# Optimization experiments

Measured on AMD Instinct MI355X. Metric: run time of the kernel, lower is better.

Reference implementation:

```python
import jax, jax.numpy as jnp
import numpy as np

B, S, D, H = 2, 2048, 1024, 16
HD = D // H  # 64
SCALE = float(np.sqrt(HD))


def setup_inputs() -> dict:
    key = jax.random.key(0)
    ks = jax.random.split(key, 5)
    x = jax.random.normal(ks[0], (B, S, D), dtype=jnp.float32)
    # causal mask: 1 = attend, 0 = masked
    mask = jnp.tril(jnp.ones((S, S), dtype=jnp.int32))
    xavier = lambda k: jax.random.normal(k, (D, D), dtype=jnp.float32) * np.sqrt(2.0 / (D + D))
    return {
        "x": x,
        "mask": mask,
        "Wq": xavier(ks[1]),
        "Wk": xavier(ks[2]),
        "Wv": xavier(ks[3]),
        "Wo": xavier(ks[4]),
    }


def reference(x, mask, Wq, Wk, Wv, Wo):
    # torch Linear(bias=False): y = x @ W.T  with W of shape [out, in]
    def heads(W):
        return (x @ W.T).reshape(B, S, H, HD).transpose(0, 2, 1, 3)  # [B,H,S,HD]

    Q, K, V = heads(Wq), heads(Wk), heads(Wv)
    scores = jnp.einsum("bhqd,bhkd->bhqk", Q, K) / SCALE  # [B,H,S,S]
    scores = jnp.where(mask[None, None] == 0, -jnp.inf, scores)
    attn = jax.nn.softmax(scores, axis=-1)
    attn = jnp.where(jnp.isnan(attn), jnp.zeros_like(attn), attn)  # nan-fix for fully masked rows
    # dropout is identity in eval / p=0
    out = jnp.einsum("bhqk,bhkd->bhqd", attn, V)  # [B,H,S,HD]
    out = out.transpose(0, 2, 1, 3).reshape(B, S, D)
    return out @ Wo.T
```

## Files before the change

### kernel.cpp

```cpp
#include <hip/hip_runtime.h>


using bfx8 = __attribute__((ext_vector_type(8))) short;
using bfx4 = __attribute__((ext_vector_type(4))) short;
using fx4  = __attribute__((ext_vector_type(4))) float;

#define NB 2
#define NS 2048
#define ND 1024
#define NH 16
#define NHD 64
#define LSTR 72

__device__ __forceinline__ unsigned short f2bf(float f) {
  union { float f; unsigned u; } v; v.f = f;
  return (unsigned short)((v.u + 0x7fffu + ((v.u >> 16) & 1u)) >> 16);
}
__device__ __forceinline__ unsigned pk2(float a, float b) {
  return (unsigned)f2bf(a) | ((unsigned)f2bf(b) << 16);
}

#define GLD16(gp, lp) __builtin_amdgcn_global_load_lds( \
    (__attribute__((address_space(1))) void*)(gp),      \
    (__attribute__((address_space(3))) void*)(lp), 16, 0, 0)

__global__ __launch_bounds__(256)
void cvt_all(const float4* __restrict__ x,  const float4* __restrict__ wq,
             const float4* __restrict__ wk, const float4* __restrict__ wv,
             const float4* __restrict__ wo, unsigned short* __restrict__ dst) {
  const int NT4 = (NB * NS * ND) / 4, NW4 = (ND * ND) / 4;
  const int i = blockIdx.x * 256 + threadIdx.x;
  const float4* src;
  int off;
  if (i < NT4) {
    src = x; off = i;
  } else {
    const int k = i - NT4;
    const int seg = k / NW4;
    off = k - seg * NW4;
    src = (seg == 0) ? wq : (seg == 1) ? wk : (seg == 2) ? wv : wo;
  }
  float4 f = src[off];
  uint2 w;
  w.x = pk2(f.x, f.y);
  w.y = pk2(f.z, f.w);
  *(uint2*)(dst + (size_t)i * 4) = w;
}

template <bool BF16>
__global__ __launch_bounds__(256)
void gemm_qkv(const void* __restrict__ xv,
              const void* __restrict__ W0v, const void* __restrict__ W1v,
              const void* __restrict__ W2v,
              unsigned short* __restrict__ Qb, unsigned short* __restrict__ Kb,
              unsigned short* __restrict__ Vt, float SCL) {
  __shared__ __attribute__((aligned(16))) unsigned short As[128 * 32];
  __shared__ __attribute__((aligned(16))) unsigned short Bs[128 * 32];
  const int t = threadIdx.x;
  const int lane = t & 63, wave = t >> 6;
  const int wr = wave >> 1, wc = wave & 1;
  const int r16 = lane & 15, quad = lane >> 4;
  const int m0 = blockIdx.x * 128, n0 = blockIdx.y * 128;
  const int z = blockIdx.z;
  const void* Wv = (z == 0) ? W0v : (z == 1) ? W1v : W2v;
  const int KD = 1024;
  fx4 acc[4][4] = {};
  const int row2 = t >> 1, kh = t & 1;
  const int c0 = t, c1 = t + 256;

  for (int k0 = 0; k0 < KD; k0 += 32) {
    if constexpr (BF16) {
      const unsigned short* A = (const unsigned short*)xv;
      const unsigned short* W = (const unsigned short*)Wv;
      GLD16(A + (size_t)(m0 + (c0 >> 2)) * KD + (size_t)(c0 & 3) * 8 + k0, &As[c0 * 8]);
      GLD16(A + (size_t)(m0 + (c1 >> 2)) * KD + (size_t)(c1 & 3) * 8 + k0, &As[c1 * 8]);
      GLD16(W + (size_t)(n0 + (c0 >> 2)) * KD + (size_t)(c0 & 3) * 8 + k0, &Bs[c0 * 8]);
      GLD16(W + (size_t)(n0 + (c1 >> 2)) * KD + (size_t)(c1 & 3) * 8 + k0, &Bs[c1 * 8]);
    } else {
      const float* A = (const float*)xv;
      const float* W = (const float*)Wv;
      {
        const float4* src = (const float4*)(A + (size_t)(m0 + row2) * KD + k0 + kh * 16);
        float4 f0 = src[0], f1 = src[1], f2 = src[2], f3 = src[3];
        uint4 w0 = {pk2(f0.x, f0.y), pk2(f0.z, f0.w), pk2(f1.x, f1.y), pk2(f1.z, f1.w)};
        uint4 w1 = {pk2(f2.x, f2.y), pk2(f2.z, f2.w), pk2(f3.x, f3.y), pk2(f3.z, f3.w)};
        *(uint4*)&As[row2 * 32 + kh * 16] = w0;
        *(uint4*)&As[row2 * 32 + kh * 16 + 8] = w1;
      }
      {
        const float4* src = (const float4*)(W + (size_t)(n0 + row2) * KD + k0 + kh * 16);
        float4 f0 = src[0], f1 = src[1], f2 = src[2], f3 = src[3];
        uint4 w0 = {pk2(f0.x, f0.y), pk2(f0.z, f0.w), pk2(f1.x, f1.y), pk2(f1.z, f1.w)};
        uint4 w1 = {pk2(f2.x, f2.y), pk2(f2.z, f2.w), pk2(f3.x, f3.y), pk2(f3.z, f3.w)};
        *(uint4*)&Bs[row2 * 32 + kh * 16] = w0;
        *(uint4*)&Bs[row2 * 32 + kh * 16 + 8] = w1;
      }
    }
    __syncthreads();
    bfx8 af[4], bfr[4];
#pragma unroll
    for (int mt = 0; mt < 4; mt++)
      af[mt] = *(const bfx8*)&As[(wr * 64 + mt * 16 + r16) * 32 + quad * 8];
#pragma unroll
    for (int nt = 0; nt < 4; nt++)
      bfr[nt] = *(const bfx8*)&Bs[(wc * 64 + nt * 16 + r16) * 32 + quad * 8];
#pragma unroll
    for (int mt = 0; mt < 4; mt++)
#pragma unroll
      for (int nt = 0; nt < 4; nt++)
        acc[mt][nt] = __builtin_amdgcn_mfma_f32_16x16x32_bf16(
            af[mt], bfr[nt], acc[mt][nt], 0, 0, 0);
    __syncthreads();
  }
#pragma unroll
  for (int mt = 0; mt < 4; mt++) {
#pragma unroll
    for (int nt = 0; nt < 4; nt++) {
      fx4 v = acc[mt][nt];
      const int mb = m0 + wr * 64 + mt * 16 + quad * 4;
      const int n = n0 + wc * 64 + nt * 16 + r16;
      const int b = mb >> 11, s = mb & (NS - 1);
      const int h = n >> 6, hd = n & (NHD - 1);
      if (z <= 1) {
        unsigned short* C = (z == 0) ? Qb : Kb;
        const float sc = (z == 0) ? SCL : 1.0f;
        const size_t base = ((size_t)(b * NH + h) * NS + s) * NHD + hd;
#pragma unroll
        for (int r = 0; r < 4; r++) C[base + (size_t)r * NHD] = f2bf(v[r] * sc);
      } else {
        const size_t base = ((size_t)(b * NH + h) * NHD + hd) * NS + s;
        uint2 pw;
        pw.x = pk2(v[0], v[1]);
        pw.y = pk2(v[2], v[3]);
        *(uint2*)(Vt + base) = pw;
      }
    }
  }
}

template <bool BF16>
__global__ __launch_bounds__(256)
void gemm_out(const unsigned short* __restrict__ A,
              const void* __restrict__ Wv,
              float* __restrict__ C) {
  __shared__ __attribute__((aligned(16))) unsigned short As[128 * 32];
  __shared__ __attribute__((aligned(16))) unsigned short Bs[128 * 32];
  const int t = threadIdx.x;
  const int lane = t & 63, wave = t >> 6;
  const int wr = wave >> 1, wc = wave & 1;
  const int r16 = lane & 15, quad = lane >> 4;
  const int m0 = blockIdx.x * 128, n0 = blockIdx.y * 128;
  const int KD = 1024;
  fx4 acc[4][4] = {};
  const int row2 = t >> 1, kh = t & 1;
  const int c0 = t, c1 = t + 256;
  for (int k0 = 0; k0 < KD; k0 += 32) {
    GLD16(A + (size_t)(m0 + (c0 >> 2)) * KD + (size_t)(c0 & 3) * 8 + k0, &As[c0 * 8]);
    GLD16(A + (size_t)(m0 + (c1 >> 2)) * KD + (size_t)(c1 & 3) * 8 + k0, &As[c1 * 8]);
    if constexpr (BF16) {
      const unsigned short* W = (const unsigned short*)Wv;
      GLD16(W + (size_t)(n0 + (c0 >> 2)) * KD + (size_t)(c0 & 3) * 8 + k0, &Bs[c0 * 8]);
      GLD16(W + (size_t)(n0 + (c1 >> 2)) * KD + (size_t)(c1 & 3) * 8 + k0, &Bs[c1 * 8]);
    } else {
      const float* W = (const float*)Wv;
      const float4* src = (const float4*)(W + (size_t)(n0 + row2) * KD + k0 + kh * 16);
      float4 f0 = src[0], f1 = src[1], f2 = src[2], f3 = src[3];
      uint4 w0 = {pk2(f0.x, f0.y), pk2(f0.z, f0.w), pk2(f1.x, f1.y), pk2(f1.z, f1.w)};
      uint4 w1 = {pk2(f2.x, f2.y), pk2(f2.z, f2.w), pk2(f3.x, f3.y), pk2(f3.z, f3.w)};
      *(uint4*)&Bs[row2 * 32 + kh * 16] = w0;
      *(uint4*)&Bs[row2 * 32 + kh * 16 + 8] = w1;
    }
    __syncthreads();
    bfx8 af[4], bfr[4];
#pragma unroll
    for (int mt = 0; mt < 4; mt++)
      af[mt] = *(const bfx8*)&As[(wr * 64 + mt * 16 + r16) * 32 + quad * 8];
#pragma unroll
    for (int nt = 0; nt < 4; nt++)
      bfr[nt] = *(const bfx8*)&Bs[(wc * 64 + nt * 16 + r16) * 32 + quad * 8];
#pragma unroll
    for (int mt = 0; mt < 4; mt++)
#pragma unroll
      for (int nt = 0; nt < 4; nt++)
        acc[mt][nt] = __builtin_amdgcn_mfma_f32_16x16x32_bf16(
            af[mt], bfr[nt], acc[mt][nt], 0, 0, 0);
    __syncthreads();
  }
#pragma unroll
  for (int mt = 0; mt < 4; mt++) {
#pragma unroll
    for (int nt = 0; nt < 4; nt++) {
      fx4 v = acc[mt][nt];
      const int s = m0 + wr * 64 + mt * 16 + quad * 4;
      const int n = n0 + wc * 64 + nt * 16 + r16;
      const size_t base = (size_t)s * ND + n;
#pragma unroll
      for (int r = 0; r < 4; r++) C[base + (size_t)r * ND] = v[r];
    }
  }
}

__global__ __launch_bounds__(256)
void attn_mfma(const unsigned short* __restrict__ Q,
               const unsigned short* __restrict__ K,
               const unsigned short* __restrict__ Vt,
               unsigned short* __restrict__ O) {
  __shared__ __attribute__((aligned(16))) unsigned short Ks[64 * LSTR];
  __shared__ __attribute__((aligned(16))) unsigned short Vs[64 * LSTR];
  const int t = threadIdx.x;
  const int lane = t & 63, wave = t >> 6;
  const int r16 = lane & 15, quad = lane >> 4;
  const int bh = blockIdx.x;
  const int j = blockIdx.y;
  const int tile = (j < 8) ? j : 23 - j;
  const int b = bh >> 4, h = bh & (NH - 1);
  const int q0b = tile * 128;
  const int q0w = q0b + wave * 32;
  const int nT = (q0b + 128) >> 6;
  const unsigned short* Qp = Q + (size_t)bh * NS * NHD;
  const unsigned short* Kp = K + (size_t)bh * NS * NHD;
  const unsigned short* Vp = Vt + (size_t)bh * NHD * NS;

  bfx8 qf[2][2];
#pragma unroll
  for (int qt = 0; qt < 2; qt++)
#pragma unroll
    for (int hs = 0; hs < 2; hs++)
      qf[qt][hs] = *(const bfx8*)&Qp[(size_t)(q0w + qt * 16 + r16) * NHD + hs * 32 + quad * 8];

  fx4 acc[2][4] = {};
  float lsum[2] = {0.0f, 0.0f};

  const int c0 = t, c1 = t + 256;
  uint4 kr0 = *(const uint4*)&Kp[0 * 64 + 8 * c0];
  uint4 kr1 = *(const uint4*)&Kp[0 * 64 + 8 * c1];
  uint4 vr0 = *(const uint4*)&Vp[(size_t)(c0 >> 3) * NS + 0 + (c0 & 7) * 8];
  uint4 vr1 = *(const uint4*)&Vp[(size_t)(c1 >> 3) * NS + 0 + (c1 & 7) * 8];

  for (int tt = 0; tt < nT; tt++) {
    __syncthreads();
    *(uint4*)&Ks[(c0 >> 3) * LSTR + (c0 & 7) * 8] = kr0;
    *(uint4*)&Ks[(c1 >> 3) * LSTR + (c1 & 7) * 8] = kr1;
    *(uint4*)&Vs[(c0 >> 3) * LSTR + (c0 & 7) * 8] = vr0;
    *(uint4*)&Vs[(c1 >> 3) * LSTR + (c1 & 7) * 8] = vr1;
    if (tt + 1 < nT) {
      const int kk = (tt + 1) * 64;
      kr0 = *(const uint4*)&Kp[kk * 64 + 8 * c0];
      kr1 = *(const uint4*)&Kp[kk * 64 + 8 * c1];
      vr0 = *(const uint4*)&Vp[(size_t)(c0 >> 3) * NS + kk + (c0 & 7) * 8];
      vr1 = *(const uint4*)&Vp[(size_t)(c1 >> 3) * NS + kk + (c1 & 7) * 8];
    }
    __syncthreads();

#pragma unroll
    for (int ks32 = 0; ks32 < 2; ks32++) {
      const int kkeff = tt * 64 + ks32 * 32;
      if (kkeff > q0w) break;
      bfx8 kf[2][2];
      bfx4 vf[4][2];
#pragma unroll
      for (int kt = 0; kt < 2; kt++)
#pragma unroll
        for (int hs = 0; hs < 2; hs++)
          kf[kt][hs] = *(const bfx8*)&Ks[(ks32 * 32 + kt * 16 + r16) * LSTR + hs * 32 + quad * 8];
#pragma unroll
      for (int mt = 0; mt < 4; mt++)
#pragma unroll
        for (int ks = 0; ks < 2; ks++)
          vf[mt][ks] = *(const bfx4*)&Vs[(mt * 16 + r16) * LSTR + ks32 * 32 + ks * 16 + quad * 4];

      fx4 st[2][2] = {};
#pragma unroll
      for (int kt = 0; kt < 2; kt++)
#pragma unroll
        for (int qt = 0; qt < 2; qt++)
#pragma unroll
          for (int hs = 0; hs < 2; hs++)
            st[kt][qt] = __builtin_amdgcn_mfma_f32_16x16x32_bf16(
                kf[kt][hs], qf[qt][hs], st[kt][qt], 0, 0, 0);

      if (kkeff == q0w) {
#pragma unroll
        for (int kt = 0; kt < 2; kt++)
#pragma unroll
          for (int qt = 0; qt < 2; qt++) {
            const int query = q0w + qt * 16 + r16;
#pragma unroll
            for (int r = 0; r < 4; r++) {
              const int key = kkeff + kt * 16 + quad * 4 + r;
              if (key > query) st[kt][qt][r] = -1e30f;
            }
          }
      }

#pragma unroll
      for (int qt = 0; qt < 2; qt++) {
        float p[2][4];
        float ps = 0.0f;
#pragma unroll
        for (int kt = 0; kt < 2; kt++)
#pragma unroll
          for (int r = 0; r < 4; r++) {
            p[kt][r] = exp2f(st[kt][qt][r]);
            ps += p[kt][r];
          }
        lsum[qt] += ps;
        uint4 pbu;
        pbu.x = pk2(p[0][0], p[0][1]);
        pbu.y = pk2(p[0][2], p[0][3]);
        pbu.z = pk2(p[1][0], p[1][1]);
        pbu.w = pk2(p[1][2], p[1][3]);
        bfx8 pb = *(bfx8*)&pbu;
#pragma unroll
        for (int mt = 0; mt < 4; mt++) {
          bfx8 va = __builtin_shufflevector(vf[mt][0], vf[mt][1], 0, 1, 2, 3, 4, 5, 6, 7);
          acc[qt][mt] = __builtin_amdgcn_mfma_f32_16x16x32_bf16(
              va, pb, acc[qt][mt], 0, 0, 0);
        }
      }
    }
  }

#pragma unroll
  for (int qt = 0; qt < 2; qt++) {
    float l = lsum[qt];
    l += __shfl_xor(l, 16);
    l += __shfl_xor(l, 32);
    const float rinv = 1.0f / l;
    const int s = q0w + qt * 16 + r16;
#pragma unroll
    for (int mt = 0; mt < 4; mt++) {
      const int d = h * NHD + mt * 16 + quad * 4;
      uint2 pw;
      pw.x = pk2(acc[qt][mt][0] * rinv, acc[qt][mt][1] * rinv);
      pw.y = pk2(acc[qt][mt][2] * rinv, acc[qt][mt][3] * rinv);
      *(uint2*)(O + ((size_t)b * NS + s) * ND + d) = pw;
    }
  }
}

extern "C" void kernel_launch(void* const* d_in, const int* in_sizes, int n_in,
                              void* d_out, int out_size, void* d_ws, size_t ws_size,
                              hipStream_t stream) {
  const float* x  = (const float*)d_in[0];
  const float* Wq = (const float*)d_in[2];
  const float* Wk = (const float*)d_in[3];
  const float* Wv = (const float*)d_in[4];
  const float* Wo = (const float*)d_in[5];
  float* out = (float*)d_out;
  unsigned short* ws = (unsigned short*)d_ws;
  const float QSCL = 0.125f * 1.44269504f;
  dim3 blk(256);
  const size_t NT = (size_t)NB * NS * ND;
  const size_t NW = (size_t)ND * ND;

  if (ws_size >= (size_t)48 * 1024 * 1024) {
    unsigned short* xb  = ws;
    unsigned short* Wqb = ws + NT;
    unsigned short* Wkb = ws + NT + NW;
    unsigned short* Wvb = ws + NT + 2 * NW;
    unsigned short* Wob = ws + NT + 3 * NW;
    unsigned short* Qb  = ws + NT + 4 * NW;
    unsigned short* Kb  = Qb + NT;
    unsigned short* Vt  = Qb + 2 * NT;
    unsigned short* Ob  = Qb + 3 * NT;
    const int total4 = (int)((NT + 4 * NW) / 4);
    hipLaunchKernelGGL(cvt_all, dim3(total4 / 256), blk, 0, stream,
                       (const float4*)x, (const float4*)Wq, (const float4*)Wk,
                       (const float4*)Wv, (const float4*)Wo, xb);
    hipLaunchKernelGGL((gemm_qkv<true>), dim3(32, 8, 3), blk, 0, stream,
                       xb, Wqb, Wkb, Wvb, Qb, Kb, Vt, QSCL);
    hipLaunchKernelGGL(attn_mfma, dim3(32, 16), blk, 0, stream, Qb, Kb, Vt, Ob);
    hipLaunchKernelGGL((gemm_out<true>), dim3(32, 8), blk, 0, stream, Ob, Wob, out);
  } else if (ws_size >= (size_t)32 * 1024 * 1024) {
    unsigned short* Qb = ws;
    unsigned short* Kb = ws + NT;
    unsigned short* Vt = ws + 2 * NT;
    unsigned short* Ob = ws + 3 * NT;
    hipLaunchKernelGGL((gemm_qkv<false>), dim3(32, 8, 3), blk, 0, stream,
                       x, Wq, Wk, Wv, Qb, Kb, Vt, QSCL);
    hipLaunchKernelGGL(attn_mfma, dim3(32, 16), blk, 0, stream, Qb, Kb, Vt, Ob);
    hipLaunchKernelGGL((gemm_out<false>), dim3(32, 8), blk, 0, stream, Ob, Wo, out);
  } else {
    const size_t NBA = (size_t)NS * ND;
    unsigned short* Qb = ws;
    unsigned short* Kb = ws + NBA;
    unsigned short* Vt = ws + 2 * NBA;
    unsigned short* Ob = ws + 3 * NBA;
    for (int b = 0; b < NB; b++) {
      const float* xb = x + (size_t)b * NS * ND;
      float* ob = out + (size_t)b * NS * ND;
      hipLaunchKernelGGL((gemm_qkv<false>), dim3(16, 8, 3), blk, 0, stream,
                         xb, Wq, Wk, Wv, Qb, Kb, Vt, QSCL);
      hipLaunchKernelGGL(attn_mfma, dim3(16, 16), blk, 0, stream, Qb, Kb, Vt, Ob);
      hipLaunchKernelGGL((gemm_out<false>), dim3(16, 8), blk, 0, stream, Ob, Wo, ob);
    }
  }
}
```

Baseline: 215.4 us.

## Transpose QKV GEMM over concatenated weights, truncate P to bf16, reorder attention tiles

The QKV projection becomes a single GEMM over the concatenated bf16 weights (which are already contiguous in the workspace), computing W·xᵀ so that each lane's four accumulator values run along the feature dimension. This lets Q and K be written as packed 8-byte stores instead of scattered scalar stores. The attention kernel now schedules query tiles heaviest-first and packs the probabilities to bf16 by truncation instead of round-to-nearest, which saves ALU work but adds a small rounding bias. The fp32 fallback path is split into its own kernel with unchanged logic.

```diff
diff --git a/kernel.cpp b/kernel.cpp
--- a/kernel.cpp
+++ b/kernel.cpp
@@ -18,6 +18,10 @@
 }
 __device__ __forceinline__ unsigned pk2(float a, float b) {
   return (unsigned)f2bf(a) | ((unsigned)f2bf(b) << 16);
+}
+__device__ __forceinline__ unsigned pkt(float a, float b) {
+  union { float f; unsigned u; } ua, ub; ua.f = a; ub.f = b;
+  return (ua.u >> 16) | (ub.u & 0xffff0000u);
 }
 
 #define GLD16(gp, lp) __builtin_amdgcn_global_load_lds( \
@@ -47,13 +51,84 @@
   *(uint2*)(dst + (size_t)i * 4) = w;
 }
 
-template <bool BF16>
 __global__ __launch_bounds__(256)
-void gemm_qkv(const void* __restrict__ xv,
-              const void* __restrict__ W0v, const void* __restrict__ W1v,
-              const void* __restrict__ W2v,
-              unsigned short* __restrict__ Qb, unsigned short* __restrict__ Kb,
-              unsigned short* __restrict__ Vt, float SCL) {
+void gemm_qkvT(const unsigned short* __restrict__ Wcat,
+               const unsigned short* __restrict__ xb,
+               unsigned short* __restrict__ Qb, unsigned short* __restrict__ Kb,
+               unsigned short* __restrict__ Vt, float SCL) {
+  __shared__ __attribute__((aligned(16))) unsigned short As[128 * 32];
+  __shared__ __attribute__((aligned(16))) unsigned short Bs[128 * 32];
+  const int t = threadIdx.x;
+  const int lane = t & 63, wave = t >> 6;
+  const int wr = wave >> 1, wc = wave & 1;
+  const int r16 = lane & 15, quad = lane >> 4;
+  const int n0 = blockIdx.x * 128;
+  const int m0 = blockIdx.y * 128;
+  const int KD = 1024;
+  fx4 acc[4][4] = {};
+  const int c0 = t, c1 = t + 256;
+
+  for (int k0 = 0; k0 < KD; k0 += 32) {
+    GLD16(Wcat + (size_t)(n0 + (c0 >> 2)) * KD + (size_t)(c0 & 3) * 8 + k0, &As[c0 * 8]);
+    GLD16(Wcat + (size_t)(n0 + (c1 >> 2)) * KD + (size_t)(c1 & 3) * 8 + k0, &As[c1 * 8]);
+    GLD16(xb   + (size_t)(m0 + (c0 >> 2)) * KD + (size_t)(c0 & 3) * 8 + k0, &Bs[c0 * 8]);
+    GLD16(xb   + (size_t)(m0 + (c1 >> 2)) * KD + (size_t)(c1 & 3) * 8 + k0, &Bs[c1 * 8]);
+    __syncthreads();
+    bfx8 af[4], bfr[4];
+#pragma unroll
+    for (int ni = 0; ni < 4; ni++)
+      af[ni] = *(const bfx8*)&As[(wr * 64 + ni * 16 + r16) * 32 + quad * 8];
+#pragma unroll
+    for (int mi = 0; mi < 4; mi++)
+      bfr[mi] = *(const bfx8*)&Bs[(wc * 64 + mi * 16 + r16) * 32 + quad * 8];
+#pragma unroll
+    for (int ni = 0; ni < 4; ni++)
+#pragma unroll
+      for (int mi = 0; mi < 4; mi++)
+        acc[ni][mi] = __builtin_amdgcn_mfma_f32_16x16x32_bf16(
+            af[ni], bfr[mi], acc[ni][mi], 0, 0, 0);
+    __syncthreads();
+  }
+#pragma unroll
+  for (int ni = 0; ni < 4; ni++) {
+#pragma unroll
+    for (int mi = 0; mi < 4; mi++) {
+      fx4 v = acc[ni][mi];
+      const int n = n0 + wr * 64 + ni * 16 + quad * 4;
+      const int m = m0 + wc * 64 + mi * 16 + r16;
+      const int b = m >> 11, s = m & (NS - 1);
+      if (n0 < 1024) {
+        const int h = n >> 6, hd = n & (NHD - 1);
+        const size_t base = ((size_t)(b * NH + h) * NS + s) * NHD + hd;
+        uint2 pw;
+        pw.x = pk2(v[0] * SCL, v[1] * SCL);
+        pw.y = pk2(v[2] * SCL, v[3] * SCL);
+        *(uint2*)(Qb + base) = pw;
+      } else if (n0 < 2048) {
+        const int n2 = n - 1024;
+        const int h = n2 >> 6, hd = n2 & (NHD - 1);
+        const size_t base = ((size_t)(b * NH + h) * NS + s) * NHD + hd;
+        uint2 pw;
+        pw.x = pk2(v[0], v[1]);
+        pw.y = pk2(v[2], v[3]);
+        *(uint2*)(Kb + base) = pw;
+      } else {
+        const int n2 = n - 2048;
+        const int h = n2 >> 6, hd = n2 & (NHD - 1);
+        const size_t base = ((size_t)(b * NH + h) * NHD + hd) * NS + s;
+#pragma unroll
+        for (int r = 0; r < 4; r++) Vt[base + (size_t)r * NS] = f2bf(v[r]);
+      }
+    }
+  }
+}
+
+__global__ __launch_bounds__(256)
+void gemm_qkv_f32(const float* __restrict__ x,
+                  const float* __restrict__ W0, const float* __restrict__ W1,
+                  const float* __restrict__ W2,
+                  unsigned short* __restrict__ Qb, unsigned short* __restrict__ Kb,
+                  unsigned short* __restrict__ Vt, float SCL) {
   __shared__ __attribute__((aligned(16))) unsigned short As[128 * 32];
   __shared__ __attribute__((aligned(16))) unsigned short Bs[128 * 32];
   const int t = threadIdx.x;
@@ -62,39 +137,26 @@
   const int r16 = lane & 15, quad = lane >> 4;
   const int m0 = blockIdx.x * 128, n0 = blockIdx.y * 128;
   const int z = blockIdx.z;
-  const void* Wv = (z == 0) ? W0v : (z == 1) ? W1v : W2v;
+  const float* W = (z == 0) ? W0 : (z == 1) ? W1 : W2;
   const int KD = 1024;
   fx4 acc[4][4] = {};
   const int row2 = t >> 1, kh = t & 1;
-  const int c0 = t, c1 = t + 256;
-
   for (int k0 = 0; k0 < KD; k0 += 32) {
-    if constexpr (BF16) {
-      const unsigned short* A = (const unsigned short*)xv;
-      const unsigned short* W = (const unsigned short*)Wv;
-      GLD16(A + (size_t)(m0 + (c0 >> 2)) * KD + (size_t)(c0 & 3) * 8 + k0, &As[c0 * 8]);
-      GLD16(A + (size_t)(m0 + (c1 >> 2)) * KD + (size_t)(c1 & 3) * 8 + k0, &As[c1 * 8]);
-      GLD16(W + (size_t)(n0 + (c0 >> 2)) * KD + (size_t)(c0 & 3) * 8 + k0, &Bs[c0 * 8]);
-      GLD16(W + (size_t)(n0 + (c1 >> 2)) * KD + (size_t)(c1 & 3) * 8 + k0, &Bs[c1 * 8]);
-    } else {
-      const float* A = (const float*)xv;
-      const float* W = (const float*)Wv;
-      {
-        const float4* src = (const float4*)(A + (size_t)(m0 + row2) * KD + k0 + kh * 16);
-        float4 f0 = src[0], f1 = src[1], f2 = src[2], f3 = src[3];
-        uint4 w0 = {pk2(f0.x, f0.y), pk2(f0.z, f0.w), pk2(f1.x, f1.y), pk2(f1.z, f1.w)};
-        uint4 w1 = {pk2(f2.x, f2.y), pk2(f2.z, f2.w), pk2(f3.x, f3.y), pk2(f3.z, f3.w)};
-        *(uint4*)&As[row2 * 32 + kh * 16] = w0;
-        *(uint4*)&As[row2 * 32 + kh * 16 + 8] = w1;
-      }
-      {
-        const float4* src = (const float4*)(W + (size_t)(n0 + row2) * KD + k0 + kh * 16);
-        float4 f0 = src[0], f1 = src[1], f2 = src[2], f3 = src[3];
-        uint4 w0 = {pk2(f0.x, f0.y), pk2(f0.z, f0.w), pk2(f1.x, f1.y), pk2(f1.z, f1.w)};
-        uint4 w1 = {pk2(f2.x, f2.y), pk2(f2.z, f2.w), pk2(f3.x, f3.y), pk2(f3.z, f3.w)};
-        *(uint4*)&Bs[row2 * 32 + kh * 16] = w0;
-        *(uint4*)&Bs[row2 * 32 + kh * 16 + 8] = w1;
-      }
+    {
+      const float4* src = (const float4*)(x + (size_t)(m0 + row2) * KD + k0 + kh * 16);
+      float4 f0 = src[0], f1 = src[1], f2 = src[2], f3 = src[3];
+      uint4 w0 = {pk2(f0.x, f0.y), pk2(f0.z, f0.w), pk2(f1.x, f1.y), pk2(f1.z, f1.w)};
+      uint4 w1 = {pk2(f2.x, f2.y), pk2(f2.z, f2.w), pk2(f3.x, f3.y), pk2(f3.z, f3.w)};
+      *(uint4*)&As[row2 * 32 + kh * 16] = w0;
+      *(uint4*)&As[row2 * 32 + kh * 16 + 8] = w1;
+    }
+    {
+      const float4* src = (const float4*)(W + (size_t)(n0 + row2) * KD + k0 + kh * 16);
+      float4 f0 = src[0], f1 = src[1], f2 = src[2], f3 = src[3];
+      uint4 w0 = {pk2(f0.x, f0.y), pk2(f0.z, f0.w), pk2(f1.x, f1.y), pk2(f1.z, f1.w)};
+      uint4 w1 = {pk2(f2.x, f2.y), pk2(f2.z, f2.w), pk2(f3.x, f3.y), pk2(f3.z, f3.w)};
+      *(uint4*)&Bs[row2 * 32 + kh * 16] = w0;
+      *(uint4*)&Bs[row2 * 32 + kh * 16 + 8] = w1;
     }
     __syncthreads();
     bfx8 af[4], bfr[4];
@@ -211,8 +273,7 @@
   const int lane = t & 63, wave = t >> 6;
   const int r16 = lane & 15, quad = lane >> 4;
   const int bh = blockIdx.x;
-  const int j = blockIdx.y;
-  const int tile = (j < 8) ? j : 23 - j;
+  const int tile = 15 - blockIdx.y;
   const int b = bh >> 4, h = bh & (NH - 1);
   const int q0b = tile * 128;
   const int q0w = q0b + wave * 32;
@@ -232,10 +293,10 @@
   float lsum[2] = {0.0f, 0.0f};
 
   const int c0 = t, c1 = t + 256;
-  uint4 kr0 = *(const uint4*)&Kp[0 * 64 + 8 * c0];
-  uint4 kr1 = *(const uint4*)&Kp[0 * 64 + 8 * c1];
-  uint4 vr0 = *(const uint4*)&Vp[(size_t)(c0 >> 3) * NS + 0 + (c0 & 7) * 8];
-  uint4 vr1 = *(const uint4*)&Vp[(size_t)(c1 >> 3) * NS + 0 + (c1 & 7) * 8];
+  uint4 kr0 = *(const uint4*)&Kp[8 * c0];
+  uint4 kr1 = *(const uint4*)&Kp[8 * c1];
+  uint4 vr0 = *(const uint4*)&Vp[(size_t)(c0 >> 3) * NS + (c0 & 7) * 8];
+  uint4 vr1 = *(const uint4*)&Vp[(size_t)(c1 >> 3) * NS + (c1 & 7) * 8];
 
   for (int tt = 0; tt < nT; tt++) {
     __syncthreads();
@@ -306,10 +367,10 @@
           }
         lsum[qt] += ps;
         uint4 pbu;
-        pbu.x = pk2(p[0][0], p[0][1]);
-        pbu.y = pk2(p[0][2], p[0][3]);
-        pbu.z = pk2(p[1][0], p[1][1]);
-        pbu.w = pk2(p[1][2], p[1][3]);
+        pbu.x = pkt(p[0][0], p[0][1]);
+        pbu.y = pkt(p[0][2], p[0][3]);
+        pbu.z = pkt(p[1][0], p[1][1]);
+        pbu.w = pkt(p[1][2], p[1][3]);
         bfx8 pb = *(bfx8*)&pbu;
 #pragma unroll
         for (int mt = 0; mt < 4; mt++) {
@@ -355,21 +416,19 @@
   const size_t NW = (size_t)ND * ND;
 
   if (ws_size >= (size_t)48 * 1024 * 1024) {
-    unsigned short* xb  = ws;
-    unsigned short* Wqb = ws + NT;
-    unsigned short* Wkb = ws + NT + NW;
-    unsigned short* Wvb = ws + NT + 2 * NW;
-    unsigned short* Wob = ws + NT + 3 * NW;
-    unsigned short* Qb  = ws + NT + 4 * NW;
-    unsigned short* Kb  = Qb + NT;
-    unsigned short* Vt  = Qb + 2 * NT;
-    unsigned short* Ob  = Qb + 3 * NT;
+    unsigned short* xb   = ws;
+    unsigned short* Wcat = ws + NT;
+    unsigned short* Wob  = ws + NT + 3 * NW;
+    unsigned short* Qb   = ws + NT + 4 * NW;
+    unsigned short* Kb   = Qb + NT;
+    unsigned short* Vt   = Qb + 2 * NT;
+    unsigned short* Ob   = Qb + 3 * NT;
     const int total4 = (int)((NT + 4 * NW) / 4);
     hipLaunchKernelGGL(cvt_all, dim3(total4 / 256), blk, 0, stream,
                        (const float4*)x, (const float4*)Wq, (const float4*)Wk,
                        (const float4*)Wv, (const float4*)Wo, xb);
-    hipLaunchKernelGGL((gemm_qkv<true>), dim3(32, 8, 3), blk, 0, stream,
-                       xb, Wqb, Wkb, Wvb, Qb, Kb, Vt, QSCL);
+    hipLaunchKernelGGL(gemm_qkvT, dim3(24, 32), blk, 0, stream,
+                       Wcat, xb, Qb, Kb, Vt, QSCL);
     hipLaunchKernelGGL(attn_mfma, dim3(32, 16), blk, 0, stream, Qb, Kb, Vt, Ob);
     hipLaunchKernelGGL((gemm_out<true>), dim3(32, 8), blk, 0, stream, Ob, Wob, out);
   } else if (ws_size >= (size_t)32 * 1024 * 1024) {
@@ -377,7 +436,7 @@
     unsigned short* Kb = ws + NT;
     unsigned short* Vt = ws + 2 * NT;
     unsigned short* Ob = ws + 3 * NT;
-    hipLaunchKernelGGL((gemm_qkv<false>), dim3(32, 8, 3), blk, 0, stream,
+    hipLaunchKernelGGL(gemm_qkv_f32, dim3(32, 8, 3), blk, 0, stream,
                        x, Wq, Wk, Wv, Qb, Kb, Vt, QSCL);
     hipLaunchKernelGGL(attn_mfma, dim3(32, 16), blk, 0, stream, Qb, Kb, Vt, Ob);
     hipLaunchKernelGGL((gemm_out<false>), dim3(32, 8), blk, 0, stream, Ob, Wo, out);
@@ -390,7 +449,7 @@
     for (int b = 0; b < NB; b++) {
       const float* xb = x + (size_t)b * NS * ND;
       float* ob = out + (size_t)b * NS * ND;
-      hipLaunchKernelGGL((gemm_qkv<false>), dim3(16, 8, 3), blk, 0, stream,
+      hipLaunchKernelGGL(gemm_qkv_f32, dim3(16, 8, 3), blk, 0, stream,
                          xb, Wq, Wk, Wv, Qb, Kb, Vt, QSCL);
       hipLaunchKernelGGL(attn_mfma, dim3(16, 16), blk, 0, stream, Qb, Kb, Vt, Ob);
       hipLaunchKernelGGL((gemm_out<false>), dim3(16, 8), blk, 0, stream, Ob, Wo, ob);
```

Result: faster. 201.5 us (-6.5%).
